# Kernel optimization log

Measured on AMD Instinct MI355X. Metric: run time of the kernel, lower is better.

## Reference

```python
import jax, jax.numpy as jnp
import numpy as np

HEADS = 16
EMBED_SIZE = 1024
HEAD_OUT = EMBED_SIZE // HEADS  # 64
B, T = 4, 2048


def setup_inputs() -> dict:
    key = jax.random.key(0)
    ks = jax.random.split(key, 7)
    std = 0.02
    return {
        "embeddings": jax.random.normal(ks[0], (B, T, EMBED_SIZE), dtype=jnp.float32),
        "Wq": jax.random.normal(ks[1], (HEAD_OUT, EMBED_SIZE), dtype=jnp.float32) * std,
        "bq": jax.random.normal(ks[2], (HEAD_OUT,), dtype=jnp.float32) * std,
        "Wk": jax.random.normal(ks[3], (HEAD_OUT, EMBED_SIZE), dtype=jnp.float32) * std,
        "bk": jax.random.normal(ks[4], (HEAD_OUT,), dtype=jnp.float32) * std,
        "Wv": jax.random.normal(ks[5], (HEAD_OUT, EMBED_SIZE), dtype=jnp.float32) * std,
        "bv": jax.random.normal(ks[6], (HEAD_OUT,), dtype=jnp.float32) * std,
    }


def reference(embeddings, Wq, bq, Wk, bk, Wv, bv):
    b, t, c = embeddings.shape
    x = embeddings.reshape(b * t, c)  # (BT, C) - original flattens batch+seq
    q = x @ Wq.T + bq  # (BT, head_out)
    k = x @ Wk.T + bk
    v = x @ Wv.T + bv
    scale = jnp.asarray(c, dtype=x.dtype) ** 0.5  # scaled by embed_size, not head_dim
    att = jax.nn.softmax((q @ k.T) / scale, axis=-1)  # (BT, BT) cross-batch attention
    y = (att @ v).reshape(b, t, -1)  # (B, T, head_out)
    # Every head uses the same shared q/k/v Linear, so all head outputs are identical;
    # the original loop concatenates the same result HEADS times.
    return jnp.tile(y, (1, 1, HEADS))  # (B, T, C)
```

## Files before the change

### kernel.cpp

```cpp
#include <hip/hip_runtime.h>
#include <stdint.h>

#define TOK 8192
#define EMB 1024
#define HD 64
#define HEADS 16
#define KVBLK 64

typedef float f32x4 __attribute__((ext_vector_type(4)));
typedef short s16x8 __attribute__((ext_vector_type(8)));

__device__ __forceinline__ unsigned short f2bf(float f) {
    unsigned u = __float_as_uint(f);
    unsigned r = (u + 0x7FFFu + ((u >> 16) & 1u)) >> 16;
    return (unsigned short)r;
}

__device__ __forceinline__ unsigned cvt_pk_bf16(float lo, float hi) {
    unsigned r;
    asm("v_cvt_pk_bf16_f32 %0, %1, %2" : "=v"(r) : "v"(lo), "v"(hi));
    return r;
}

__device__ __forceinline__ s16x8 frag4(unsigned a, unsigned b, unsigned c, unsigned d) {
    int4 t = make_int4((int)a, (int)b, (int)c, (int)d);
    return __builtin_bit_cast(s16x8, t);
}

__global__ __launch_bounds__(256) void prep_kernel(
        const float* __restrict__ Wq, const float* __restrict__ bq,
        const float* __restrict__ Wk, const float* __restrict__ bk,
        const float* __restrict__ Wv, const float* __restrict__ bv,
        unsigned short* __restrict__ wb, float* __restrict__ bb) {
    int gid = blockIdx.x * 256 + threadIdx.x;
    int row = gid >> 10, col = gid & 1023;
    const float QS = 1.4426950408889634f / 32.0f;
    float w;
    if (row < 64)       w = Wq[row * 1024 + col] * QS;
    else if (row < 128) w = Wk[(row - 64) * 1024 + col];
    else                w = Wv[(row - 128) * 1024 + col];
    wb[gid] = f2bf(w);
    if (gid < 192) {
        float b;
        if (gid < 64)       b = bq[gid] * QS;
        else if (gid < 128) b = bk[gid - 64];
        else                b = bv[gid - 128];
        bb[gid] = b;
    }
}

#define XPAD 1040
__global__ __launch_bounds__(768) void proj_kernel(
        const float* __restrict__ x, const unsigned short* __restrict__ wb,
        const float* __restrict__ bb,
        unsigned short* __restrict__ qw, unsigned char* __restrict__ kimg,
        unsigned char* __restrict__ vimg) {
    __shared__ __align__(16) unsigned short xb[16][XPAD];
    int tid = threadIdx.x;
    int row0 = blockIdx.x * 16;

    if (tid < 512) {
        #pragma unroll
        for (int i = 0; i < 8; ++i) {
            int flat = i * 2048 + tid * 4;
            int r = flat >> 10, col = flat & 1023;
            float4 f = *(const float4*)(x + (size_t)(row0 + r) * EMB + col);
            uint2 p;
            p.x = cvt_pk_bf16(f.x, f.y);
            p.y = cvt_pk_bf16(f.z, f.w);
            *(uint2*)(&xb[r][col]) = p;
        }
    }
    __syncthreads();

    int wave = tid >> 6;
    int lane = tid & 63;
    int c = lane & 15, g = lane >> 4;

    f32x4 acc = {};
    const unsigned short* bp0 = wb + (size_t)(wave * 16 + c) * EMB;
    #pragma unroll 8
    for (int ks = 0; ks < EMB / 32; ++ks) {
        s16x8 a = *(const s16x8*)(&xb[c][ks * 32 + g * 8]);
        s16x8 b = *(const s16x8*)(bp0 + ks * 32 + g * 8);
        acc = __builtin_amdgcn_mfma_f32_16x16x32_bf16(a, b, acc, 0, 0, 0);
    }
    float bias = bb[wave * 16 + c];
    acc[0] += bias; acc[1] += bias; acc[2] += bias; acc[3] += bias;

    size_t tile = (size_t)(row0 >> 6);
    int tI = (row0 >> 4) & 3;

    if (wave < 4) {
        int col = wave * 16 + c;
        #pragma unroll
        for (int r = 0; r < 4; ++r)
            qw[(size_t)(row0 + g * 4 + r) * HD + col] = f2bf(acc[r]);
    } else if (wave < 8) {
        int wv = wave - 4;
        int C = wv * 16 + c;
        int kh = C >> 5;
        int gg = (C & 31) >> 3;
        int j = C & 7;
        unsigned char* base = kimg + tile * 8192 + (size_t)((kh * 4 + tI) * 1024 + j * 2);
        #pragma unroll
        for (int r = 0; r < 4; ++r) {
            int cl = g * 4 + r;
            *(unsigned short*)(base + (gg * 16 + cl) * 16) = f2bf(acc[r]);
        }
    } else {
        int t = wave - 8;
        int base16 = tI * 16 + g * 4;
        int ks = base16 >> 5;
        int s = (base16 >> 3) & 3;
        int gg = ((s & 1) << 1) | (s >> 1);
        int j0 = base16 & 7;
        uint2 pack;
        pack.x = cvt_pk_bf16(acc[0], acc[1]);
        pack.y = cvt_pk_bf16(acc[2], acc[3]);
        *(uint2*)(vimg + tile * 8192 +
                  (size_t)((ks * 4 + t) * 1024 + (gg * 16 + c) * 16 + j0 * 2)) = pack;
    }
}

template <int S>
__global__ __launch_bounds__(256, 2) void attn_kernel(
        const unsigned short* __restrict__ qw, const unsigned char* __restrict__ kimg,
        const unsigned char* __restrict__ vimg,
        float* __restrict__ po, float* __restrict__ pl) {
    constexpr int KVS = TOK / S;
    constexpr int NIT = KVS / KVBLK;
    constexpr int QB = TOK / 256;
    __shared__ __align__(16) unsigned char lds[2][16384];
    int wave = threadIdx.x >> 6;
    int lane = threadIdx.x & 63;
    int c = lane & 15, g = lane >> 4;
    int qb = blockIdx.x % QB;
    int split = blockIdx.x / QB;
    int wq0 = qb * 256 + wave * 64;
    int tile0 = split * NIT;
    bool odd = (g & 1) != 0;

    s16x8 aq[4][2];
    #pragma unroll
    for (int qt = 0; qt < 4; ++qt)
        #pragma unroll
        for (int kh = 0; kh < 2; ++kh)
            aq[qt][kh] = *(const s16x8*)(qw + (size_t)(wq0 + qt * 16 + c) * HD + kh * 32 + g * 8);

    f32x4 o[4][4] = {};
    float l[4] = {};

    auto stage = [&](int buf, int tile) {
        const unsigned char* kg = kimg + (size_t)tile * 8192;
        const unsigned char* vg = vimg + (size_t)tile * 8192;
        #pragma unroll
        for (int j = 0; j < 2; ++j) {
            int off = (j * 4 + wave) * 1024;
            __builtin_amdgcn_global_load_lds(
                (const __attribute__((address_space(1))) void*)(kg + off + lane * 16),
                (__attribute__((address_space(3))) void*)(&lds[buf][off]), 16, 0, 0);
            __builtin_amdgcn_global_load_lds(
                (const __attribute__((address_space(1))) void*)(vg + off + lane * 16),
                (__attribute__((address_space(3))) void*)(&lds[buf][8192 + off]), 16, 0, 0);
        }
    };

    stage(0, tile0);
    __syncthreads();

    int buf = 0;
    #pragma unroll 1
    for (int it = 0; it < NIT; ++it) {
        int nt = (it + 1 < NIT) ? it + 1 : it;
        stage(buf ^ 1, tile0 + nt);

        const unsigned char* Kl = &lds[buf][0];
        const unsigned char* Vl = &lds[buf][8192];

        s16x8 kf[2][4];
        #pragma unroll
        for (int kh = 0; kh < 2; ++kh)
            #pragma unroll
            for (int t = 0; t < 4; ++t)
                kf[kh][t] = *(const s16x8*)(Kl + (kh * 4 + t) * 1024 + lane * 16);

        unsigned Wall[4][8];
        #pragma unroll
        for (int qp = 0; qp < 2; ++qp) {
            f32x4 st[2][4] = {};
            #pragma unroll
            for (int kh = 0; kh < 2; ++kh)
                #pragma unroll
                for (int q = 0; q < 2; ++q)
                    #pragma unroll
                    for (int t = 0; t < 4; ++t)
                        st[q][t] = __builtin_amdgcn_mfma_f32_16x16x32_bf16(
                            kf[kh][t], aq[qp * 2 + q][kh], st[q][t], 0, 0, 0);
            #pragma unroll
            for (int q = 0; q < 2; ++q) {
                int qt = qp * 2 + q;
                float p[4][4];
                #pragma unroll
                for (int t = 0; t < 4; ++t)
                    #pragma unroll
                    for (int r = 0; r < 4; ++r)
                        p[t][r] = exp2f(st[q][t][r]);
                float s0 = (p[0][0] + p[0][1]) + (p[0][2] + p[0][3]);
                float s1 = (p[1][0] + p[1][1]) + (p[1][2] + p[1][3]);
                float s2 = (p[2][0] + p[2][1]) + (p[2][2] + p[2][3]);
                float s3 = (p[3][0] + p[3][1]) + (p[3][2] + p[3][3]);
                l[qt] += (s0 + s1) + (s2 + s3);
                #pragma unroll
                for (int t = 0; t < 4; ++t) {
                    Wall[qt][t * 2 + 0] = cvt_pk_bf16(p[t][0], p[t][1]);
                    Wall[qt][t * 2 + 1] = cvt_pk_bf16(p[t][2], p[t][3]);
                }
            }
        }

        #pragma unroll
        for (int ks = 0; ks < 2; ++ks) {
            s16x8 vf[4];
            #pragma unroll
            for (int t = 0; t < 4; ++t)
                vf[t] = *(const s16x8*)(Vl + (ks * 4 + t) * 1024 + lane * 16);
            #pragma unroll
            for (int qt = 0; qt < 4; ++qt) {
                unsigned ael = Wall[qt][4 * ks + 0], aeh = Wall[qt][4 * ks + 1];
                unsigned aol = Wall[qt][4 * ks + 2], aoh = Wall[qt][4 * ks + 3];
                unsigned sl = odd ? ael : aol;
                unsigned sh = odd ? aeh : aoh;
                unsigned rl = (unsigned)__builtin_amdgcn_ds_swizzle((int)sl, 0x401F);
                unsigned rh = (unsigned)__builtin_amdgcn_ds_swizzle((int)sh, 0x401F);
                unsigned f0 = odd ? rl : ael;
                unsigned f1 = odd ? rh : aeh;
                unsigned f2 = odd ? aol : rl;
                unsigned f3 = odd ? aoh : rh;
                s16x8 pa = frag4(f0, f1, f2, f3);
                #pragma unroll
                for (int t = 0; t < 4; ++t)
                    o[qt][t] = __builtin_amdgcn_mfma_f32_16x16x32_bf16(pa, vf[t], o[qt][t], 0, 0, 0);
            }
        }
        __syncthreads();
        buf ^= 1;
    }

    #pragma unroll
    for (int qt = 0; qt < 4; ++qt) {
        #pragma unroll
        for (int t = 0; t < 4; ++t)
            #pragma unroll
            for (int r = 0; r < 4; ++r)
                po[((size_t)split * TOK + wq0 + qt * 16 + g * 4 + r) * HD + t * 16 + c] = o[qt][t][r];
        float v = l[qt];
        v += __shfl_xor(v, 16);
        v += __shfl_xor(v, 32);
        if (g == 0)
            pl[split * TOK + wq0 + qt * 16 + c] = v;
    }
}

template <int S>
__global__ __launch_bounds__(256) void combine_kernel(
        const float* __restrict__ po, const float* __restrict__ pl,
        float* __restrict__ out) {
    int gid = blockIdx.x * 256 + threadIdx.x;
    int row = gid >> 4;
    int dc = (gid & 15) * 4;
    float4 acc = {0.f, 0.f, 0.f, 0.f};
    float denom = 0.f;
    #pragma unroll
    for (int s = 0; s < S; ++s) {
        denom += pl[s * TOK + row];
        float4 p = *(const float4*)(po + ((size_t)s * TOK + row) * HD + dc);
        acc.x += p.x; acc.y += p.y; acc.z += p.z; acc.w += p.w;
    }
    float inv = 1.0f / denom;
    acc.x *= inv; acc.y *= inv; acc.z *= inv; acc.w *= inv;
    #pragma unroll
    for (int h = 0; h < HEADS; ++h)
        *(float4*)(out + (size_t)row * EMB + h * HD + dc) = acc;
}

extern "C" void kernel_launch(void* const* d_in, const int* in_sizes, int n_in,
                              void* d_out, int out_size, void* d_ws, size_t ws_size,
                              hipStream_t stream) {
    const float* x  = (const float*)d_in[0];
    const float* Wq = (const float*)d_in[1];
    const float* bq = (const float*)d_in[2];
    const float* Wk = (const float*)d_in[3];
    const float* bk = (const float*)d_in[4];
    const float* Wv = (const float*)d_in[5];
    const float* bv = (const float*)d_in[6];
    float* out = (float*)d_out;
    char* ws = (char*)d_ws;
    unsigned short* wb   = (unsigned short*)(ws + 0x000000);
    float*          bb   = (float*)         (ws + 0x060000);
    unsigned short* qw   = (unsigned short*)(ws + 0x061000);
    unsigned char*  kimg = (unsigned char*) (ws + 0x161000);
    unsigned char*  vimg = (unsigned char*) (ws + 0x261000);
    float*          po   = (float*)         (ws + 0x361000);

    prep_kernel<<<dim3(768), dim3(256), 0, stream>>>(Wq, bq, Wk, bk, Wv, bv, wb, bb);
    proj_kernel<<<dim3(512), dim3(768), 0, stream>>>(x, wb, bb, qw, kimg, vimg);

    const size_t base = 0x361000;
    const size_t per_split = (size_t)TOK * HD * 4;
    const size_t per_pl    = (size_t)TOK * 4;
    auto need = [&](int s) { return base + (size_t)s * (per_split + per_pl); };

    if (ws_size >= need(16)) {
        float* pl = (float*)(ws + base + 16 * per_split);
        attn_kernel<16><<<dim3(32 * 16), dim3(256), 0, stream>>>(qw, kimg, vimg, po, pl);
        combine_kernel<16><<<dim3(512), dim3(256), 0, stream>>>(po, pl, out);
    } else {
        float* pl = (float*)(ws + base + 8 * per_split);
        attn_kernel<8><<<dim3(32 * 8), dim3(256), 0, stream>>>(qw, kimg, vimg, po, pl);
        combine_kernel<8><<<dim3(512), dim3(256), 0, stream>>>(po, pl, out);
    }
}
```

Before: 162.6 us.

## Halve queries per wave in attention and split projection K-loop into two accumulators

The attention kernel now gives each wave 32 query rows instead of 64. This doubles the grid to 64 query blocks per split and raises the occupancy hint to 3 blocks per CU. The intent is more parallelism and less register pressure, at the cost of loading each K/V tile twice as often per query. The projection kernel also splits its 32-step MFMA reduction into two independent accumulators to break the dependency chain, then sums them with the bias.

Result: faster. 151.2 us (-7.0%).

```diff
diff --git a/kernel.cpp b/kernel.cpp
--- a/kernel.cpp
+++ b/kernel.cpp
@@ -77,16 +77,23 @@
     int lane = tid & 63;
     int c = lane & 15, g = lane >> 4;
 
-    f32x4 acc = {};
+    f32x4 acc0 = {}, acc1 = {};
     const unsigned short* bp0 = wb + (size_t)(wave * 16 + c) * EMB;
     #pragma unroll 8
-    for (int ks = 0; ks < EMB / 32; ++ks) {
-        s16x8 a = *(const s16x8*)(&xb[c][ks * 32 + g * 8]);
-        s16x8 b = *(const s16x8*)(bp0 + ks * 32 + g * 8);
-        acc = __builtin_amdgcn_mfma_f32_16x16x32_bf16(a, b, acc, 0, 0, 0);
+    for (int ks = 0; ks < 16; ++ks) {
+        s16x8 a0 = *(const s16x8*)(&xb[c][ks * 32 + g * 8]);
+        s16x8 b0 = *(const s16x8*)(bp0 + ks * 32 + g * 8);
+        acc0 = __builtin_amdgcn_mfma_f32_16x16x32_bf16(a0, b0, acc0, 0, 0, 0);
+        s16x8 a1 = *(const s16x8*)(&xb[c][(ks + 16) * 32 + g * 8]);
+        s16x8 b1 = *(const s16x8*)(bp0 + (ks + 16) * 32 + g * 8);
+        acc1 = __builtin_amdgcn_mfma_f32_16x16x32_bf16(a1, b1, acc1, 0, 0, 0);
     }
     float bias = bb[wave * 16 + c];
-    acc[0] += bias; acc[1] += bias; acc[2] += bias; acc[3] += bias;
+    f32x4 acc;
+    acc[0] = acc0[0] + acc1[0] + bias;
+    acc[1] = acc0[1] + acc1[1] + bias;
+    acc[2] = acc0[2] + acc1[2] + bias;
+    acc[3] = acc0[3] + acc1[3] + bias;
 
     size_t tile = (size_t)(row0 >> 6);
     int tI = (row0 >> 4) & 3;
@@ -124,32 +131,32 @@
 }
 
 template <int S>
-__global__ __launch_bounds__(256, 2) void attn_kernel(
+__global__ __launch_bounds__(256, 3) void attn_kernel(
         const unsigned short* __restrict__ qw, const unsigned char* __restrict__ kimg,
         const unsigned char* __restrict__ vimg,
         float* __restrict__ po, float* __restrict__ pl) {
     constexpr int KVS = TOK / S;
     constexpr int NIT = KVS / KVBLK;
-    constexpr int QB = TOK / 256;
+    constexpr int QB = TOK / 128;
     __shared__ __align__(16) unsigned char lds[2][16384];
     int wave = threadIdx.x >> 6;
     int lane = threadIdx.x & 63;
     int c = lane & 15, g = lane >> 4;
     int qb = blockIdx.x % QB;
     int split = blockIdx.x / QB;
-    int wq0 = qb * 256 + wave * 64;
+    int wq0 = qb * 128 + wave * 32;
     int tile0 = split * NIT;
     bool odd = (g & 1) != 0;
 
-    s16x8 aq[4][2];
+    s16x8 aq[2][2];
     #pragma unroll
-    for (int qt = 0; qt < 4; ++qt)
+    for (int qt = 0; qt < 2; ++qt)
         #pragma unroll
         for (int kh = 0; kh < 2; ++kh)
             aq[qt][kh] = *(const s16x8*)(qw + (size_t)(wq0 + qt * 16 + c) * HD + kh * 32 + g * 8);
 
-    f32x4 o[4][4] = {};
-    float l[4] = {};
+    f32x4 o[2][4] = {};
+    float l[2] = {};
 
     auto stage = [&](int buf, int tile) {
         const unsigned char* kg = kimg + (size_t)tile * 8192;
@@ -185,37 +192,34 @@
             for (int t = 0; t < 4; ++t)
                 kf[kh][t] = *(const s16x8*)(Kl + (kh * 4 + t) * 1024 + lane * 16);
 
-        unsigned Wall[4][8];
-        #pragma unroll
-        for (int qp = 0; qp < 2; ++qp) {
-            f32x4 st[2][4] = {};
-            #pragma unroll
-            for (int kh = 0; kh < 2; ++kh)
-                #pragma unroll
-                for (int q = 0; q < 2; ++q)
-                    #pragma unroll
-                    for (int t = 0; t < 4; ++t)
-                        st[q][t] = __builtin_amdgcn_mfma_f32_16x16x32_bf16(
-                            kf[kh][t], aq[qp * 2 + q][kh], st[q][t], 0, 0, 0);
-            #pragma unroll
-            for (int q = 0; q < 2; ++q) {
-                int qt = qp * 2 + q;
-                float p[4][4];
+        f32x4 st[2][4] = {};
+        #pragma unroll
+        for (int kh = 0; kh < 2; ++kh)
+            #pragma unroll
+            for (int q = 0; q < 2; ++q)
                 #pragma unroll
                 for (int t = 0; t < 4; ++t)
-                    #pragma unroll
-                    for (int r = 0; r < 4; ++r)
-                        p[t][r] = exp2f(st[q][t][r]);
-                float s0 = (p[0][0] + p[0][1]) + (p[0][2] + p[0][3]);
-                float s1 = (p[1][0] + p[1][1]) + (p[1][2] + p[1][3]);
-                float s2 = (p[2][0] + p[2][1]) + (p[2][2] + p[2][3]);
-                float s3 = (p[3][0] + p[3][1]) + (p[3][2] + p[3][3]);
-                l[qt] += (s0 + s1) + (s2 + s3);
+                    st[q][t] = __builtin_amdgcn_mfma_f32_16x16x32_bf16(
+                        kf[kh][t], aq[q][kh], st[q][t], 0, 0, 0);
+
+        unsigned Wall[2][8];
+        #pragma unroll
+        for (int q = 0; q < 2; ++q) {
+            float p[4][4];
+            #pragma unroll
+            for (int t = 0; t < 4; ++t)
                 #pragma unroll
-                for (int t = 0; t < 4; ++t) {
-                    Wall[qt][t * 2 + 0] = cvt_pk_bf16(p[t][0], p[t][1]);
-                    Wall[qt][t * 2 + 1] = cvt_pk_bf16(p[t][2], p[t][3]);
-                }
+                for (int r = 0; r < 4; ++r)
+                    p[t][r] = exp2f(st[q][t][r]);
+            float s0 = (p[0][0] + p[0][1]) + (p[0][2] + p[0][3]);
+            float s1 = (p[1][0] + p[1][1]) + (p[1][2] + p[1][3]);
+            float s2 = (p[2][0] + p[2][1]) + (p[2][2] + p[2][3]);
+            float s3 = (p[3][0] + p[3][1]) + (p[3][2] + p[3][3]);
+            l[q] += (s0 + s1) + (s2 + s3);
+            #pragma unroll
+            for (int t = 0; t < 4; ++t) {
+                Wall[q][t * 2 + 0] = cvt_pk_bf16(p[t][0], p[t][1]);
+                Wall[q][t * 2 + 1] = cvt_pk_bf16(p[t][2], p[t][3]);
             }
         }
 
@@ -226,7 +230,7 @@
             for (int t = 0; t < 4; ++t)
                 vf[t] = *(const s16x8*)(Vl + (ks * 4 + t) * 1024 + lane * 16);
             #pragma unroll
-            for (int qt = 0; qt < 4; ++qt) {
+            for (int qt = 0; qt < 2; ++qt) {
                 unsigned ael = Wall[qt][4 * ks + 0], aeh = Wall[qt][4 * ks + 1];
                 unsigned aol = Wall[qt][4 * ks + 2], aoh = Wall[qt][4 * ks + 3];
                 unsigned sl = odd ? ael : aol;
@@ -248,7 +252,7 @@
     }
 
     #pragma unroll
-    for (int qt = 0; qt < 4; ++qt) {
+    for (int qt = 0; qt < 2; ++qt) {
         #pragma unroll
         for (int t = 0; t < 4; ++t)
             #pragma unroll
@@ -313,11 +317,11 @@
 
     if (ws_size >= need(16)) {
         float* pl = (float*)(ws + base + 16 * per_split);
-        attn_kernel<16><<<dim3(32 * 16), dim3(256), 0, stream>>>(qw, kimg, vimg, po, pl);
+        attn_kernel<16><<<dim3(64 * 16), dim3(256), 0, stream>>>(qw, kimg, vimg, po, pl);
         combine_kernel<16><<<dim3(512), dim3(256), 0, stream>>>(po, pl, out);
     } else {
         float* pl = (float*)(ws + base + 8 * per_split);
-        attn_kernel<8><<<dim3(32 * 8), dim3(256), 0, stream>>>(qw, kimg, vimg, po, pl);
+        attn_kernel<8><<<dim3(64 * 8), dim3(256), 0, stream>>>(qw, kimg, vimg, po, pl);
         combine_kernel<8><<<dim3(512), dim3(256), 0, stream>>>(po, pl, out);
     }
 }
```
